# Optimization experiments

Measured on AMD Instinct MI355X. Metric: run time of the kernel, lower is better.

The kernel has to match this reference:

```python
import jax, jax.numpy as jnp
import numpy as np


def setup_inputs() -> dict:
    key = jax.random.key(0)
    k1, k2 = jax.random.split(key)
    B, L = 16384, 2048
    v = jax.random.normal(k1, (B, L), dtype=jnp.float32)
    z = jax.random.normal(k2, (B, L), dtype=jnp.float32)
    return {"v": v, "z": z}


def reference(v, z):
    # Householder reflection per batch row:
    #   z_new = z - 2 * v (v^T z) / ||v||^2
    # The original torch code builds the [B, L, L] outer product v v^T via bmm;
    # this is mathematically identical to the O(B*L) form below.
    vz = jnp.sum(v * z, axis=1, keepdims=True)       # [B, 1]  v . z
    norm_sq = jnp.sum(v * v, axis=1, keepdims=True)  # [B, 1]  ||v||^2
    return z - 2.0 * v * (vz / norm_sq)
```

## Files before the change

### kernel.cpp

```cpp
#include <hip/hip_runtime.h>


#define ROW_LEN 2048
#define BLOCK 256
#define WAVES (BLOCK / 64)

typedef float v4f __attribute__((ext_vector_type(4)));

__global__ __launch_bounds__(BLOCK) void householder_row_kernel(
    const float* __restrict__ v,
    const float* __restrict__ z,
    float* __restrict__ out)
{
    const int row = blockIdx.x;
    const size_t base = (size_t)row * ROW_LEN;
    const int t = threadIdx.x;

    const v4f* v4 = reinterpret_cast<const v4f*>(v + base);
    const v4f* z4 = reinterpret_cast<const v4f*>(z + base);
    v4f* o4 = reinterpret_cast<v4f*>(out + base);

    v4f va = v4[t];
    v4f vb = __builtin_nontemporal_load(&v4[t + BLOCK]);
    v4f za = z4[t];
    v4f zb = z4[t + BLOCK];

    float vz = va.x * za.x + va.y * za.y + va.z * za.z + va.w * za.w
             + vb.x * zb.x + vb.y * zb.y + vb.z * zb.z + vb.w * zb.w;
    float vv = va.x * va.x + va.y * va.y + va.z * va.z + va.w * va.w
             + vb.x * vb.x + vb.y * vb.y + vb.z * vb.z + vb.w * vb.w;

    #pragma unroll
    for (int off = 32; off > 0; off >>= 1) {
        vz += __shfl_down(vz, off);
        vv += __shfl_down(vv, off);
    }

    __shared__ float svz[WAVES];
    __shared__ float svv[WAVES];

    const int wave = t >> 6;
    const int lane = t & 63;
    if (lane == 0) { svz[wave] = vz; svv[wave] = vv; }
    __syncthreads();

    float tvz = 0.f, tvv = 0.f;
    #pragma unroll
    for (int w = 0; w < WAVES; ++w) { tvz += svz[w]; tvv += svv[w]; }
    const float s = 2.0f * tvz / tvv;

    v4f oa = za - s * va;
    v4f ob = zb - s * vb;

    __builtin_nontemporal_store(oa, &o4[t]);
    __builtin_nontemporal_store(ob, &o4[t + BLOCK]);
}

extern "C" void kernel_launch(void* const* d_in, const int* in_sizes, int n_in,
                              void* d_out, int out_size, void* d_ws, size_t ws_size,
                              hipStream_t stream) {
    const float* v = (const float*)d_in[0];
    const float* z = (const float*)d_in[1];
    float* out = (float*)d_out;

    const int B = in_sizes[0] / ROW_LEN;
    householder_row_kernel<<<B, BLOCK, 0, stream>>>(v, z, out);
}
```

Baseline: 61.12 us.

## Assign one row per wavefront to drop shared-memory block reduction

Each 64-lane wavefront now processes a full 2048-float row, holding 8 float4 of v and z per lane, and a block covers four rows. The row reduction finishes with xor shuffles alone, so the LDS exchange and __syncthreads are gone. The cost is more registers per thread and fewer blocks, which can reduce memory-level parallelism or occupancy in this bandwidth-bound kernel. The nontemporal load hint on v is also dropped.

After: 61.73 us. Within noise of the previous version (+1.0%).

```diff
diff --git a/kernel.cpp b/kernel.cpp
--- a/kernel.cpp
+++ b/kernel.cpp
@@ -3,7 +3,8 @@
 
 #define ROW_LEN 2048
 #define BLOCK 256
-#define WAVES (BLOCK / 64)
+#define ROWS_PER_BLOCK 4
+#define V4_PER_LANE 8
 
 typedef float v4f __attribute__((ext_vector_type(4)));
 
@@ -12,48 +13,44 @@
     const float* __restrict__ z,
     float* __restrict__ out)
 {
-    const int row = blockIdx.x;
+    const int wave = threadIdx.x >> 6;
+    const int lane = threadIdx.x & 63;
+    const int row = blockIdx.x * ROWS_PER_BLOCK + wave;
     const size_t base = (size_t)row * ROW_LEN;
-    const int t = threadIdx.x;
 
     const v4f* v4 = reinterpret_cast<const v4f*>(v + base);
     const v4f* z4 = reinterpret_cast<const v4f*>(z + base);
     v4f* o4 = reinterpret_cast<v4f*>(out + base);
 
-    v4f va = v4[t];
-    v4f vb = __builtin_nontemporal_load(&v4[t + BLOCK]);
-    v4f za = z4[t];
-    v4f zb = z4[t + BLOCK];
+    v4f vr[V4_PER_LANE], zr[V4_PER_LANE];
+    #pragma unroll
+    for (int k = 0; k < V4_PER_LANE; ++k) {
+        vr[k] = v4[lane + k * 64];
+        zr[k] = z4[lane + k * 64];
+    }
 
-    float vz = va.x * za.x + va.y * za.y + va.z * za.z + va.w * za.w
-             + vb.x * zb.x + vb.y * zb.y + vb.z * zb.z + vb.w * zb.w;
-    float vv = va.x * va.x + va.y * va.y + va.z * va.z + va.w * va.w
-             + vb.x * vb.x + vb.y * vb.y + vb.z * vb.z + vb.w * vb.w;
+    float vz = 0.f, vv = 0.f;
+    #pragma unroll
+    for (int k = 0; k < V4_PER_LANE; ++k) {
+        vz += vr[k].x * zr[k].x + vr[k].y * zr[k].y
+            + vr[k].z * zr[k].z + vr[k].w * zr[k].w;
+        vv += vr[k].x * vr[k].x + vr[k].y * vr[k].y
+            + vr[k].z * vr[k].z + vr[k].w * vr[k].w;
+    }
 
     #pragma unroll
     for (int off = 32; off > 0; off >>= 1) {
-        vz += __shfl_down(vz, off);
-        vv += __shfl_down(vv, off);
+        vz += __shfl_xor(vz, off);
+        vv += __shfl_xor(vv, off);
     }
 
-    __shared__ float svz[WAVES];
-    __shared__ float svv[WAVES];
+    const float s = 2.0f * vz / vv;
 
-    const int wave = t >> 6;
-    const int lane = t & 63;
-    if (lane == 0) { svz[wave] = vz; svv[wave] = vv; }
-    __syncthreads();
-
-    float tvz = 0.f, tvv = 0.f;
     #pragma unroll
-    for (int w = 0; w < WAVES; ++w) { tvz += svz[w]; tvv += svv[w]; }
-    const float s = 2.0f * tvz / tvv;
-
-    v4f oa = za - s * va;
-    v4f ob = zb - s * vb;
-
-    __builtin_nontemporal_store(oa, &o4[t]);
-    __builtin_nontemporal_store(ob, &o4[t + BLOCK]);
+    for (int k = 0; k < V4_PER_LANE; ++k) {
+        v4f o = zr[k] - s * vr[k];
+        __builtin_nontemporal_store(o, &o4[lane + k * 64]);
+    }
 }
 
 extern "C" void kernel_launch(void* const* d_in, const int* in_sizes, int n_in,
@@ -64,5 +61,6 @@
     float* out = (float*)d_out;
 
     const int B = in_sizes[0] / ROW_LEN;
-    householder_row_kernel<<<B, BLOCK, 0, stream>>>(v, z, out);
+    const int grid = B / ROWS_PER_BLOCK;
+    householder_row_kernel<<<grid, BLOCK, 0, stream>>>(v, z, out);
 }
```
